# Kernel optimization log

Measured on AMD Instinct MI355X. Metric: run time of the kernel, lower is better.

The kernel has to match this reference:

```python
import jax, jax.numpy as jnp
import numpy as np

N_NODES = 100000
N_EDGES = 1600000
D_IN = 64
D_OUT = 64
ROW_WINDOW = 16  # TCGNN row-window size (metadata only)


def setup_inputs() -> dict:
    key = jax.random.key(0)
    ks = jax.random.split(key, 7)
    X = jax.random.normal(ks[0], (N_NODES, D_IN), dtype=jnp.float32)
    weights = jax.random.normal(ks[1], (D_IN, D_OUT), dtype=jnp.float32)
    # CSR row pointers: sorted offsets into the edge list, endpoints pinned.
    rp = jnp.sort(jax.random.randint(ks[2], (N_NODES + 1,), 0, N_EDGES, dtype=jnp.int32))
    row_pointers = rp.at[0].set(0).at[-1].set(N_EDGES)
    column_index = jax.random.randint(ks[3], (N_EDGES,), 0, N_NODES, dtype=jnp.int32)
    # TCGNN tiling metadata (does not affect the math; kept for signature fidelity)
    blockPartition = jax.random.randint(ks[4], (N_NODES // ROW_WINDOW,), 0, 8, dtype=jnp.int32)
    edgeToColumn = jax.random.randint(ks[5], (N_EDGES,), 0, N_NODES, dtype=jnp.int32)
    edgeToRow = jax.random.randint(ks[6], (N_EDGES,), 0, N_NODES, dtype=jnp.int32)
    return {
        "X": X,
        "weights": weights,
        "row_pointers": row_pointers,
        "column_index": column_index,
        "blockPartition": blockPartition,
        "edgeToColumn": edgeToColumn,
        "edgeToRow": edgeToRow,
    }


def reference(X, weights, row_pointers, column_index, blockPartition, edgeToColumn, edgeToRow):
    # TCGNN.forward == unweighted CSR SpMM: X_prime[i] = sum_{j in N(i)} X[j]
    n_edges = column_index.shape[0]
    # Map each edge position to its CSR row id.
    row_ids = jnp.searchsorted(row_pointers, jnp.arange(n_edges, dtype=row_pointers.dtype), side="right") - 1
    gathered = X[column_index]  # [n_edges, d_in] irregular gather
    X_prime = jax.ops.segment_sum(gathered, row_ids, num_segments=X.shape[0])  # [n_nodes, d_in]
    return X_prime @ weights  # dense GEMM [n_nodes, d_out]
```

## Files before the change

### kernel.cpp

```cpp
#include <hip/hip_runtime.h>
#include <cstdint>
#include <cstddef>

#define D 64

typedef float    f32x4 __attribute__((ext_vector_type(4)));
typedef float    f32x2 __attribute__((ext_vector_type(2)));
typedef short    s16x8 __attribute__((ext_vector_type(8)));
typedef uint32_t u32x4 __attribute__((ext_vector_type(4)));

__device__ __forceinline__ uint32_t rne_bf16(float f) {
    uint32_t x = __float_as_uint(f);
    return (x + 0x7fffu + ((x >> 16) & 1u)) >> 16;
}
__device__ __forceinline__ float bf16lo(uint32_t u) { return __uint_as_float(u << 16); }
__device__ __forceinline__ float bf16hi(uint32_t u) { return __uint_as_float(u & 0xffff0000u); }

__global__ __launch_bounds__(256) void cast_kernel(
    const float* __restrict__ X, uint32_t* __restrict__ Xh, long n4)
{
    long i = (long)blockIdx.x * blockDim.x + threadIdx.x;
    const long stride = (long)gridDim.x * blockDim.x;
    for (; i < n4; i += stride) {
        f32x4 v = __builtin_nontemporal_load((const f32x4*)X + i);
        uint2 o;
        o.x = rne_bf16(v.x) | (rne_bf16(v.y) << 16);
        o.y = rne_bf16(v.z) | (rne_bf16(v.w) << 16);
        ((uint2*)Xh)[i] = o;
    }
}

__device__ __forceinline__ void acc_row(f32x2 acc[4], const u32x4 u) {
#pragma unroll
    for (int k = 0; k < 4; ++k) {
        f32x2 v;
        v.x = bf16lo(u[k]);
        v.y = bf16hi(u[k]);
        acc[k] += v;
    }
}

__global__ __launch_bounds__(256) void gather4_kernel(
    const uint32_t* __restrict__ Xh, const int* __restrict__ rp,
    const int* __restrict__ ci, uint32_t* __restrict__ Agg, int n_nodes)
{
    const int lane = threadIdx.x & 63;
    const int o = lane >> 3;
    const int p = lane & 7;
    const int row = (int)((blockIdx.x * blockDim.x + threadIdx.x) >> 6);
    if (row >= n_nodes) return;

    const int e0 = rp[row];
    const int e1 = rp[row + 1];

    f32x2 accA[4] = {{0.f,0.f},{0.f,0.f},{0.f,0.f},{0.f,0.f}};
    f32x2 accB[4] = {{0.f,0.f},{0.f,0.f},{0.f,0.f},{0.f,0.f}};

    for (int e = e0; e < e1; e += 64) {
        const int rem = e1 - e;
        const int last = e1 - 1;
        {
            const int i0 = ci[min(e + o,      last)];
            const int i1 = ci[min(e + 8 + o,  last)];
            const int i2 = ci[min(e + 16 + o, last)];
            const int i3 = ci[min(e + 24 + o, last)];
            u32x4 u0 = {0,0,0,0}, u1 = {0,0,0,0}, u2 = {0,0,0,0}, u3 = {0,0,0,0};
            if (o < rem)      u0 = *(const u32x4*)(Xh + (size_t)i0 * 32 + p * 4);
            if (8 + o < rem)  u1 = *(const u32x4*)(Xh + (size_t)i1 * 32 + p * 4);
            if (16 + o < rem) u2 = *(const u32x4*)(Xh + (size_t)i2 * 32 + p * 4);
            if (24 + o < rem) u3 = *(const u32x4*)(Xh + (size_t)i3 * 32 + p * 4);
            acc_row(accA, u0); acc_row(accB, u1);
            acc_row(accA, u2); acc_row(accB, u3);
        }
        if (rem > 32) {
            const int i0 = ci[min(e + 32 + o, last)];
            const int i1 = ci[min(e + 40 + o, last)];
            const int i2 = ci[min(e + 48 + o, last)];
            const int i3 = ci[min(e + 56 + o, last)];
            u32x4 u0 = {0,0,0,0}, u1 = {0,0,0,0}, u2 = {0,0,0,0}, u3 = {0,0,0,0};
            if (32 + o < rem) u0 = *(const u32x4*)(Xh + (size_t)i0 * 32 + p * 4);
            if (40 + o < rem) u1 = *(const u32x4*)(Xh + (size_t)i1 * 32 + p * 4);
            if (48 + o < rem) u2 = *(const u32x4*)(Xh + (size_t)i2 * 32 + p * 4);
            if (56 + o < rem) u3 = *(const u32x4*)(Xh + (size_t)i3 * 32 + p * 4);
            acc_row(accA, u0); acc_row(accB, u1);
            acc_row(accA, u2); acc_row(accB, u3);
        }
    }

#pragma unroll
    for (int k = 0; k < 4; ++k) {
        f32x2 v = accA[k] + accB[k];
        v.x += __shfl_xor(v.x, 8, 64);  v.y += __shfl_xor(v.y, 8, 64);
        v.x += __shfl_xor(v.x, 16, 64); v.y += __shfl_xor(v.y, 16, 64);
        v.x += __shfl_xor(v.x, 32, 64); v.y += __shfl_xor(v.y, 32, 64);
        accA[k] = v;
    }
    if (lane < 8) {
        u32x4 w;
#pragma unroll
        for (int k = 0; k < 4; ++k)
            w[k] = rne_bf16(accA[k].x) | (rne_bf16(accA[k].y) << 16);
        *(u32x4*)(Agg + (size_t)row * 32 + p * 4) = w;
    }
}

__global__ __launch_bounds__(256) void agg_gemm_kernel(
    const uint32_t* __restrict__ Agg, const float* __restrict__ W,
    float* __restrict__ out, int n_nodes)
{
    const int lane = threadIdx.x & 63;
    const int n = lane & 15;
    const int q = lane >> 4;

    s16x8 Bf[4][2];
#pragma unroll
    for (int c = 0; c < 4; ++c)
#pragma unroll
        for (int kb = 0; kb < 2; ++kb) {
            s16x8 bfr;
#pragma unroll
            for (int j = 0; j < 8; ++j) {
                const int k = kb * 32 + q * 8 + j;
                bfr[j] = (short)rne_bf16(W[k * D + c * 16 + n]);
            }
            Bf[c][kb] = bfr;
        }

    const int n_tiles = (n_nodes + 15) / 16;
    const int gwave = (int)((blockIdx.x * blockDim.x + threadIdx.x) >> 6);
    const int nwaves = (int)((gridDim.x * blockDim.x) >> 6);

    for (int t = gwave; t < n_tiles; t += nwaves) {
        const int m0 = t * 16;
        int arow = m0 + n;
        if (arow >= n_nodes) arow = n_nodes - 1;
        const s16x8 A0 = *(const s16x8*)(Agg + (size_t)arow * 32 + q * 4);
        const s16x8 A1 = *(const s16x8*)(Agg + (size_t)arow * 32 + 16 + q * 4);

        f32x4 acc[4];
#pragma unroll
        for (int c = 0; c < 4; ++c) {
            f32x4 z = {0.f, 0.f, 0.f, 0.f};
            z = __builtin_amdgcn_mfma_f32_16x16x32_bf16(A0, Bf[c][0], z, 0, 0, 0);
            z = __builtin_amdgcn_mfma_f32_16x16x32_bf16(A1, Bf[c][1], z, 0, 0, 0);
            acc[c] = z;
        }
#pragma unroll
        for (int r = 0; r < 4; ++r) {
            const int ro = m0 + q * 4 + r;
            if (ro < n_nodes) {
#pragma unroll
                for (int c = 0; c < 4; ++c)
                    out[(size_t)ro * D + c * 16 + n] = acc[c][r];
            }
        }
    }
}

__global__ __launch_bounds__(256) void fused_kernel(
    const float* __restrict__ X, const float* __restrict__ W,
    const int* __restrict__ rp, const int* __restrict__ ci,
    float* __restrict__ out, int n_nodes)
{
    __shared__ float Wl[D * D];
    for (int i = threadIdx.x; i < D * D; i += 256) Wl[i] = W[i];
    __syncthreads();

    const int lane = threadIdx.x & 63;
    const int gwave = (int)((blockIdx.x * blockDim.x + threadIdx.x) >> 6);
    const int nwaves = (int)((gridDim.x * blockDim.x) >> 6);

    for (int row = gwave; row < n_nodes; row += nwaves) {
        int e0 = rp[row];
        int e1 = rp[row + 1];
        float acc = 0.f;
        for (int e = e0; e < e1; ++e) acc += X[ci[e] * D + lane];
        float sum = 0.f;
#pragma unroll
        for (int d = 0; d < D; ++d) {
            float a = __shfl(acc, d, 64);
            sum += a * Wl[d * D + lane];
        }
        out[row * D + lane] = sum;
    }
}

extern "C" void kernel_launch(void* const* d_in, const int* in_sizes, int n_in,
                              void* d_out, int out_size, void* d_ws, size_t ws_size,
                              hipStream_t stream)
{
    const float* X  = (const float*)d_in[0];
    const float* W  = (const float*)d_in[1];
    const int*   rp = (const int*)d_in[2];
    const int*   ci = (const int*)d_in[3];
    float* out = (float*)d_out;

    const int n_nodes = in_sizes[2] - 1;
    const size_t row_bytes = 32 * sizeof(uint32_t);
    const size_t need = 2 * (size_t)n_nodes * row_bytes;

    if (ws_size >= need) {
        uint32_t* Xh  = (uint32_t*)d_ws;
        uint32_t* Agg = (uint32_t*)((char*)d_ws + (size_t)n_nodes * row_bytes);

        const long n4 = (long)n_nodes * (D / 4);
        int cast_blocks = (int)((n4 + 255) / 256);
        if (cast_blocks > 6400) cast_blocks = 6400;
        cast_kernel<<<cast_blocks, 256, 0, stream>>>(X, Xh, n4);

        const int gather_blocks = (n_nodes + 3) / 4;
        gather4_kernel<<<gather_blocks, 256, 0, stream>>>(Xh, rp, ci, Agg, n_nodes);

        const int n_tiles = (n_nodes + 15) / 16;
        const int gemm_blocks = (n_tiles + 3) / 4;
        agg_gemm_kernel<<<gemm_blocks, 256, 0, stream>>>(Agg, W, out, n_nodes);
    } else {
        fused_kernel<<<2048, 256, 0, stream>>>(X, W, rp, ci, out, n_nodes);
    }
}
```

Baseline: 148.6 us.

## Make gather kernel persistent with software-pipelined row pointer and index prefetch

```diff
diff --git a/kernel.cpp b/kernel.cpp
--- a/kernel.cpp
+++ b/kernel.cpp
@@ -40,67 +40,109 @@
     }
 }
 
-__global__ __launch_bounds__(256) void gather4_kernel(
+__global__ __launch_bounds__(256) void gather5_kernel(
     const uint32_t* __restrict__ Xh, const int* __restrict__ rp,
     const int* __restrict__ ci, uint32_t* __restrict__ Agg, int n_nodes)
 {
     const int lane = threadIdx.x & 63;
     const int o = lane >> 3;
     const int p = lane & 7;
-    const int row = (int)((blockIdx.x * blockDim.x + threadIdx.x) >> 6);
-    if (row >= n_nodes) return;
-
-    const int e0 = rp[row];
-    const int e1 = rp[row + 1];
-
-    f32x2 accA[4] = {{0.f,0.f},{0.f,0.f},{0.f,0.f},{0.f,0.f}};
-    f32x2 accB[4] = {{0.f,0.f},{0.f,0.f},{0.f,0.f},{0.f,0.f}};
-
-    for (int e = e0; e < e1; e += 64) {
-        const int rem = e1 - e;
-        const int last = e1 - 1;
-        {
-            const int i0 = ci[min(e + o,      last)];
-            const int i1 = ci[min(e + 8 + o,  last)];
-            const int i2 = ci[min(e + 16 + o, last)];
-            const int i3 = ci[min(e + 24 + o, last)];
-            u32x4 u0 = {0,0,0,0}, u1 = {0,0,0,0}, u2 = {0,0,0,0}, u3 = {0,0,0,0};
-            if (o < rem)      u0 = *(const u32x4*)(Xh + (size_t)i0 * 32 + p * 4);
-            if (8 + o < rem)  u1 = *(const u32x4*)(Xh + (size_t)i1 * 32 + p * 4);
-            if (16 + o < rem) u2 = *(const u32x4*)(Xh + (size_t)i2 * 32 + p * 4);
-            if (24 + o < rem) u3 = *(const u32x4*)(Xh + (size_t)i3 * 32 + p * 4);
-            acc_row(accA, u0); acc_row(accB, u1);
-            acc_row(accA, u2); acc_row(accB, u3);
-        }
-        if (rem > 32) {
-            const int i0 = ci[min(e + 32 + o, last)];
-            const int i1 = ci[min(e + 40 + o, last)];
-            const int i2 = ci[min(e + 48 + o, last)];
-            const int i3 = ci[min(e + 56 + o, last)];
-            u32x4 u0 = {0,0,0,0}, u1 = {0,0,0,0}, u2 = {0,0,0,0}, u3 = {0,0,0,0};
-            if (32 + o < rem) u0 = *(const u32x4*)(Xh + (size_t)i0 * 32 + p * 4);
-            if (40 + o < rem) u1 = *(const u32x4*)(Xh + (size_t)i1 * 32 + p * 4);
-            if (48 + o < rem) u2 = *(const u32x4*)(Xh + (size_t)i2 * 32 + p * 4);
-            if (56 + o < rem) u3 = *(const u32x4*)(Xh + (size_t)i3 * 32 + p * 4);
-            acc_row(accA, u0); acc_row(accB, u1);
-            acc_row(accA, u2); acc_row(accB, u3);
-        }
-    }
-
-#pragma unroll
-    for (int k = 0; k < 4; ++k) {
-        f32x2 v = accA[k] + accB[k];
-        v.x += __shfl_xor(v.x, 8, 64);  v.y += __shfl_xor(v.y, 8, 64);
-        v.x += __shfl_xor(v.x, 16, 64); v.y += __shfl_xor(v.y, 16, 64);
-        v.x += __shfl_xor(v.x, 32, 64); v.y += __shfl_xor(v.y, 32, 64);
-        accA[k] = v;
-    }
-    if (lane < 8) {
-        u32x4 w;
-#pragma unroll
-        for (int k = 0; k < 4; ++k)
-            w[k] = rne_bf16(accA[k].x) | (rne_bf16(accA[k].y) << 16);
-        *(u32x4*)(Agg + (size_t)row * 32 + p * 4) = w;
+    const int gw = (int)((blockIdx.x * blockDim.x + threadIdx.x) >> 6);
+    const int nw = (int)((gridDim.x * blockDim.x) >> 6);
+
+    int rowC = gw;
+    if (rowC >= n_nodes) return;
+
+    int e0C = rp[rowC];
+    int e1C = rp[rowC + 1];
+    int i0C, i1C, i2C, i3C;
+    {
+        const int hi = e1C - 1;
+        i0C = ci[max(min(e0C + 0  + o, hi), 0)];
+        i1C = ci[max(min(e0C + 8  + o, hi), 0)];
+        i2C = ci[max(min(e0C + 16 + o, hi), 0)];
+        i3C = ci[max(min(e0C + 24 + o, hi), 0)];
+    }
+    int rowN = rowC + nw;
+    bool hasN = rowN < n_nodes;
+    int e0N = 0, e1N = 0;
+    if (hasN) { e0N = rp[rowN]; e1N = rp[rowN + 1]; }
+
+    for (;;) {
+        int i0N, i1N, i2N, i3N;
+        if (hasN) {
+            const int hi = e1N - 1;
+            i0N = ci[max(min(e0N + 0  + o, hi), 0)];
+            i1N = ci[max(min(e0N + 8  + o, hi), 0)];
+            i2N = ci[max(min(e0N + 16 + o, hi), 0)];
+            i3N = ci[max(min(e0N + 24 + o, hi), 0)];
+        }
+        const int rowN2 = rowN + nw;
+        const bool hasN2 = hasN && (rowN2 < n_nodes);
+        int e0N2 = 0, e1N2 = 0;
+        if (hasN2) { e0N2 = rp[rowN2]; e1N2 = rp[rowN2 + 1]; }
+
+        const int deg = e1C - e0C;
+        u32x4 u0 = {0,0,0,0}, u1 = {0,0,0,0}, u2 = {0,0,0,0}, u3 = {0,0,0,0};
+        if (o < deg)      u0 = *(const u32x4*)(Xh + (size_t)i0C * 32 + p * 4);
+        if (o + 8 < deg)  u1 = *(const u32x4*)(Xh + (size_t)i1C * 32 + p * 4);
+        if (o + 16 < deg) u2 = *(const u32x4*)(Xh + (size_t)i2C * 32 + p * 4);
+        if (o + 24 < deg) u3 = *(const u32x4*)(Xh + (size_t)i3C * 32 + p * 4);
+
+        f32x2 acc[4] = {{0.f,0.f},{0.f,0.f},{0.f,0.f},{0.f,0.f}};
+        acc_row(acc, u0); acc_row(acc, u1); acc_row(acc, u2); acc_row(acc, u3);
+
+        if (deg > 32) {
+            int e = e0C + 32;
+            for (; e + 32 <= e1C; e += 32) {
+                const int j0 = ci[e + o];
+                const int j1 = ci[e + 8 + o];
+                const int j2 = ci[e + 16 + o];
+                const int j3 = ci[e + 24 + o];
+                const u32x4 v0 = *(const u32x4*)(Xh + (size_t)j0 * 32 + p * 4);
+                const u32x4 v1 = *(const u32x4*)(Xh + (size_t)j1 * 32 + p * 4);
+                const u32x4 v2 = *(const u32x4*)(Xh + (size_t)j2 * 32 + p * 4);
+                const u32x4 v3 = *(const u32x4*)(Xh + (size_t)j3 * 32 + p * 4);
+                acc_row(acc, v0); acc_row(acc, v1);
+                acc_row(acc, v2); acc_row(acc, v3);
+            }
+            const int rem = e1C - e;
+            if (rem > 0) {
+                const int hi = e1C - 1;
+                const int j0 = ci[min(e + o, hi)];
+                const int j1 = ci[min(e + 8 + o, hi)];
+                const int j2 = ci[min(e + 16 + o, hi)];
+                const int j3 = ci[min(e + 24 + o, hi)];
+                u32x4 v0 = {0,0,0,0}, v1 = {0,0,0,0}, v2 = {0,0,0,0}, v3 = {0,0,0,0};
+                if (o < rem)      v0 = *(const u32x4*)(Xh + (size_t)j0 * 32 + p * 4);
+                if (o + 8 < rem)  v1 = *(const u32x4*)(Xh + (size_t)j1 * 32 + p * 4);
+                if (o + 16 < rem) v2 = *(const u32x4*)(Xh + (size_t)j2 * 32 + p * 4);
+                if (o + 24 < rem) v3 = *(const u32x4*)(Xh + (size_t)j3 * 32 + p * 4);
+                acc_row(acc, v0); acc_row(acc, v1);
+                acc_row(acc, v2); acc_row(acc, v3);
+            }
+        }
+
+#pragma unroll
+        for (int k = 0; k < 4; ++k) {
+            f32x2 v = acc[k];
+            v.x += __shfl_xor(v.x, 8, 64);  v.y += __shfl_xor(v.y, 8, 64);
+            v.x += __shfl_xor(v.x, 16, 64); v.y += __shfl_xor(v.y, 16, 64);
+            v.x += __shfl_xor(v.x, 32, 64); v.y += __shfl_xor(v.y, 32, 64);
+            acc[k] = v;
+        }
+        if (lane < 8) {
+            u32x4 w;
+#pragma unroll
+            for (int k = 0; k < 4; ++k)
+                w[k] = rne_bf16(acc[k].x) | (rne_bf16(acc[k].y) << 16);
+            *(u32x4*)(Agg + (size_t)rowC * 32 + p * 4) = w;
+        }
+
+        if (!hasN) break;
+        rowC = rowN; e0C = e0N; e1C = e1N;
+        i0C = i0N; i1C = i1N; i2C = i2N; i3C = i3N;
+        rowN = rowN2; hasN = hasN2; e0N = e0N2; e1N = e1N2;
     }
 }
 
@@ -208,8 +250,7 @@
         if (cast_blocks > 6400) cast_blocks = 6400;
         cast_kernel<<<cast_blocks, 256, 0, stream>>>(X, Xh, n4);
 
-        const int gather_blocks = (n_nodes + 3) / 4;
-        gather4_kernel<<<gather_blocks, 256, 0, stream>>>(Xh, rp, ci, Agg, n_nodes);
+        gather5_kernel<<<2048, 256, 0, stream>>>(Xh, rp, ci, Agg, n_nodes);
 
         const int n_tiles = (n_nodes + 15) / 16;
         const int gemm_blocks = (n_tiles + 3) / 4;
```

New measurement: 147.3 us. No clear change (-0.9%).
